# Optimization experiments

Hardware: AMD Instinct MI355X
Metric: run time of the kernel (lower is better)

## Reference

```python
import jax, jax.numpy as jnp
import numpy as np

B, N, L, H, K = 65536, 32, 8, 256, 8
RMIN, RMAX = -10.0, 10.0
MIN_BIN, MIN_SLOPE = 1e-4, 1e-4
P = 3 * K + 1  # params per feature per spline


def setup_inputs() -> dict:
    key = jax.random.key(0)
    ks = jax.random.split(key, 20)
    def rn(k, shape, s=0.05):
        return (jax.random.normal(k, shape, dtype=jnp.float32) * s)
    inp = {
        'x': jax.random.normal(ks[0], (B, N), dtype=jnp.float32),
        'sc_scale': 1.0 + rn(ks[1], (L, N)),
        'sc_shift': rn(ks[2], (L, N)),
        'W_in': rn(ks[3], (L, N, H)), 'b_in': rn(ks[4], (L, H)),
        'W1a': rn(ks[5], (L, H, H)), 'b1a': rn(ks[6], (L, H)),
        'W1b': rn(ks[7], (L, H, H)), 'b1b': rn(ks[8], (L, H)),
        'W2a': rn(ks[9], (L, H, H)), 'b2a': rn(ks[10], (L, H)),
        'W2b': rn(ks[11], (L, H, H)), 'b2b': rn(ks[12], (L, H)),
        'W_out': rn(ks[13], (L, H, N * P)), 'b_out': rn(ks[14], (L, N * P)),
        'perms': jnp.asarray(np.stack([np.random.RandomState(i).permutation(N) for i in range(L)]).astype(np.int32)),
    }
    return inp


def _conditioner(mx, Wi, bi, W1a, b1a, W1b, b1b, W2a, b2a, W2b, b2b, Wo, bo):
    # mx: [B, N] masked input -> [B, N, P] spline params
    h = mx @ Wi + bi
    r = jax.nn.relu(jax.nn.relu(h @ W1a + b1a) @ W1b + b1b)
    h = h + r
    r = jax.nn.relu(jax.nn.relu(h @ W2a + b2a) @ W2b + b2b)
    h = h + r
    h = jax.nn.relu(h)
    out = h @ Wo + bo
    return out.reshape(mx.shape[0], N, P)


def _rqs_forward(x, params):
    # x: [B, N]; params: [B, N, 3K+1]. distrax RationalQuadraticSpline forward.
    uw, uh, ud = params[..., :K], params[..., K:2 * K], params[..., 2 * K:]
    total = RMAX - RMIN
    w = jax.nn.softmax(uw, axis=-1) * (total - K * MIN_BIN) + MIN_BIN
    hgt = jax.nn.softmax(uh, axis=-1) * (total - K * MIN_BIN) + MIN_BIN
    zpad = jnp.zeros_like(w[..., :1])
    xp = RMIN + jnp.concatenate([zpad, jnp.cumsum(w, -1)], -1)   # [B,N,K+1]
    yp = RMIN + jnp.concatenate([zpad, jnp.cumsum(hgt, -1)], -1)
    offset = float(np.log(np.expm1(1.0 - MIN_SLOPE)))
    d = jax.nn.softplus(ud + offset) + MIN_SLOPE                  # [B,N,K+1]
    inside = (x > RMIN) & (x < RMAX)
    xc = jnp.clip(x, RMIN, RMAX)
    # per-element bin search (knot positions vary per element)
    idx = jnp.clip(jnp.sum((xc[..., None] >= xp).astype(jnp.int32), -1) - 1, 0, K - 1)
    g = lambda a, i: jnp.take_along_axis(a, i[..., None], -1)[..., 0]
    xk, xk1 = g(xp, idx), g(xp, idx + 1)
    yk, yk1 = g(yp, idx), g(yp, idx + 1)
    dk, dk1 = g(d, idx), g(d, idx + 1)
    bw = xk1 - xk
    bh = yk1 - yk
    s = bh / bw
    z = jnp.clip((xc - xk) / bw, 0.0, 1.0)
    zz = z * (1.0 - z)
    denom = s + (dk1 + dk - 2.0 * s) * zz
    y = yk + bh * (s * z * z + dk * zz) / denom
    ld = 2.0 * jnp.log(s) + jnp.log(dk1 * z * z + 2.0 * s * zz + dk * (1.0 - z) ** 2) - 2.0 * jnp.log(denom)
    return jnp.where(inside, y, x), jnp.where(inside, ld, 0.0)


def reference(x, sc_scale, sc_shift, W_in, b_in, W1a, b1a, W1b, b1b,
              W2a, b2a, W2b, b2b, W_out, b_out, perms):
    mask0 = (jnp.arange(N) % 2).astype(bool)  # True = identity (masked)
    logdet = jnp.zeros(x.shape[0], dtype=x.dtype)
    for i in range(L):
        # Permute
        x = x[:, perms[i]]
        # Scalar affine on all features (mask_all = all-False coupling)
        x = x * sc_scale[i] + sc_shift[i]
        logdet = logdet + jnp.sum(jnp.log(jnp.abs(sc_scale[i])))
        # RQ-spline masked coupling
        mask = mask0 if i % 2 == 0 else ~mask0
        mx = jnp.where(mask, x, 0.0)
        params = _conditioner(mx, W_in[i], b_in[i], W1a[i], b1a[i], W1b[i], b1b[i],
                              W2a[i], b2a[i], W2b[i], b2b[i], W_out[i], b_out[i])
        y, ld = _rqs_forward(x, params)
        x = jnp.where(mask, x, y)
        logdet = logdet + jnp.sum(jnp.where(mask, 0.0, ld), axis=-1)
    # standard-normal base log prob
    logp = -0.5 * jnp.sum(x * x, axis=-1) - 0.5 * N * float(np.log(2.0 * np.pi))
    return logp + logdet
```

## Files before the change

### kernel.cpp

```cpp
#include <hip/hip_runtime.h>
#include <hip/hip_bf16.h>

typedef __attribute__((ext_vector_type(8))) short bf16x8;
typedef __attribute__((ext_vector_type(16))) float f32x16;
typedef __attribute__((ext_vector_type(2))) float f32x2;

#define DEVFN __device__ __forceinline__

constexpr int NFEAT = 32, NLAYER = 8, HID = 256;
constexpr int HS  = 264;
constexpr int MXS = 40;
constexpr int XS  = 33;
constexpr int WIN_E  = 2 * 256 * 16;
constexpr int WH_E   = 16 * 256 * 16;
constexpr int WOUT_E = 16 * 512 * 16;
constexpr int LAYER_E = WIN_E + 4 * WH_E + WOUT_E;
constexpr size_t WT_BYTES = (size_t)LAYER_E * NLAYER * 2;
constexpr size_t WS_NEEDED = WT_BYTES + NLAYER * 512 * 4 + 4;

constexpr float MIN_BIN = 1e-4f, MIN_SLOPE = 1e-4f;
constexpr float SOFTPLUS_OFF = 0.5411666f;
constexpr float WSCALE = 20.0f - 8.0f * MIN_BIN;

DEVFN unsigned short bf16r(float f) {
    unsigned u = __float_as_uint(f);
    u += 0x7fffu + ((u >> 16) & 1u);
    return (unsigned short)(u >> 16);
}
#if defined(__gfx950__) && __has_builtin(__builtin_amdgcn_cvt_pk_bf16_f32)
DEVFN unsigned pack2(float a, float b) {
    auto r = __builtin_amdgcn_cvt_pk_bf16_f32(a, b);
    return __builtin_bit_cast(unsigned, r);
}
#else
DEVFN unsigned pack2(float a, float b) {
    return (unsigned)bf16r(a) | ((unsigned)bf16r(b) << 16);
}
#endif
DEVFN float bflo(unsigned v) { return __uint_as_float(v << 16); }
DEVFN float bfhi(unsigned v) { return __uint_as_float(v & 0xffff0000u); }
DEVFN float frcp(float x) { return __builtin_amdgcn_rcpf(x); }
DEVFN f32x2 vmax0(f32x2 v) {
#if __has_builtin(__builtin_elementwise_max)
    return __builtin_elementwise_max(v, (f32x2){0.f, 0.f});
#else
    return (f32x2){fmaxf(v.x, 0.f), fmaxf(v.y, 0.f)};
#endif
}

__global__ __launch_bounds__(256) void prep_kernel(
    const float* __restrict__ Win, const float* __restrict__ W1a, const float* __restrict__ W1b,
    const float* __restrict__ W2a, const float* __restrict__ W2b, const float* __restrict__ Wout,
    const float* __restrict__ bout, const float* __restrict__ scS,
    short* __restrict__ wt, float* __restrict__ bo_t, float* __restrict__ sld)
{
    __shared__ float lb[16 * 800];
    const int b = blockIdx.x, t = threadIdx.x;
    if (b < 16) {
        int l = b >> 1, ks = b & 1;
        const float* src = Win + l * 32 * 256 + ks * 16 * 256;
#pragma unroll
        for (int i = 0; i < 16; i++) { int idx = t + i * 256; lb[idx] = src[idx]; }
        __syncthreads();
        short* dst = wt + (size_t)l * LAYER_E + ks * 4096;
#pragma unroll
        for (int i = 0; i < 16; i++) {
            int o = t + i * 256; int n = o >> 4, kk = o & 15;
            dst[o] = (short)bf16r(lb[kk * 256 + n]);
        }
    } else if (b < 528) {
        int id = b - 16; int l = id >> 6, mat = (id >> 4) & 3, ks = id & 15;
        const float* mats[4] = {W1a, W1b, W2a, W2b};
        const float* src = mats[mat] + l * 65536 + ks * 16 * 256;
#pragma unroll
        for (int i = 0; i < 16; i++) { int idx = t + i * 256; lb[idx] = src[idx]; }
        __syncthreads();
        short* dst = wt + (size_t)l * LAYER_E + WIN_E + mat * WH_E + ks * 4096;
#pragma unroll
        for (int i = 0; i < 16; i++) {
            int o = t + i * 256; int n = o >> 4, kk = o & 15;
            dst[o] = (short)bf16r(lb[kk * 256 + n]);
        }
    } else if (b < 656) {
        int id = b - 528; int l = id >> 4, ks = id & 15; int par = l & 1;
        const float* src = Wout + (size_t)l * 256 * 800 + ks * 16 * 800;
        for (int k = 0; k < 16; k++)
            for (int c = t; c < 800; c += 256) lb[k * 800 + c] = src[k * 800 + c];
        __syncthreads();
        short* dst = wt + (size_t)l * LAYER_E + WIN_E + 4 * WH_E + ks * 8192;
#pragma unroll
        for (int i = 0; i < 32; i++) {
            int o = t + i * 256; int c = o >> 4, kk = o & 15;
            int u = c >> 5, p = c & 31;
            float v = (p < 25) ? lb[kk * 800 + (2 * u + par) * 25 + p] : 0.0f;
            dst[o] = (short)bf16r(v);
        }
    } else {
#pragma unroll
        for (int i = 0; i < 16; i++) {
            int idx = t + i * 256;
            int l = idx >> 9, c = idx & 511, u = c >> 5, p = c & 31;
            bo_t[idx] = (p < 25) ? bout[l * 800 + (2 * u + (l & 1)) * 25 + p] : 0.0f;
        }
        lb[t] = logf(fabsf(scS[t]));
        __syncthreads();
        for (int s = 128; s > 0; s >>= 1) { if (t < s) lb[t] += lb[t + s]; __syncthreads(); }
        if (t == 0) *sld = lb[0];
    }
}

template<int KSTEPS, int NSUB, int DEPTH>
DEVFN void gemm_flip(const short* __restrict__ wt, int ntot, int nbase,
                     const unsigned short* __restrict__ B, int bs,
                     f32x16 (&acc)[NSUB][2])
{
    constexpr int D = (KSTEPS < DEPTH) ? KSTEPS : DEPTH;
    const int lane = threadIdx.x & 63;
    const int l31 = lane & 31, l5 = lane >> 5;
    const bf16x8* __restrict__ w8 = (const bf16x8*)wt;
    const int wb = (nbase + l31) * 2 + l5;
    const int krow = ntot * 2;
    bf16x8 a[D][NSUB];
#pragma unroll
    for (int p = 0; p < D; p++)
#pragma unroll
        for (int s = 0; s < NSUB; s++) a[p][s] = w8[(size_t)p * krow + wb + s * 64];
    const unsigned short* bp = B + l31 * bs + l5 * 8;
#pragma unroll
    for (int k = 0; k < KSTEPS; k++) {
        bf16x8 b0 = *(const bf16x8*)(bp + k * 16);
        bf16x8 b1 = *(const bf16x8*)(bp + 32 * bs + k * 16);
#pragma unroll
        for (int s = 0; s < NSUB; s++) {
            acc[s][0] = __builtin_amdgcn_mfma_f32_32x32x16_bf16(a[k % D][s], b0, acc[s][0], 0, 0, 0);
            acc[s][1] = __builtin_amdgcn_mfma_f32_32x32x16_bf16(a[k % D][s], b1, acc[s][1], 0, 0, 0);
        }
        if (k + D < KSTEPS) {
#pragma unroll
            for (int s = 0; s < NSUB; s++) a[k % D][s] = w8[(size_t)(k + D) * krow + wb + s * 64];
        }
    }
}

DEVFN void binit(f32x16& a, const float* __restrict__ bias)
{
    const int q = (threadIdx.x >> 5) & 1;
    const float* bp = bias + 4 * q;
#pragma unroll
    for (int g = 0; g < 4; g++) {
        float4 b = *(const float4*)(bp + 8 * g);
        a[4*g+0] = b.x; a[4*g+1] = b.y; a[4*g+2] = b.z; a[4*g+3] = b.w;
    }
}

template<int MODE>
DEVFN void store_h(const f32x16& v, unsigned short* buf, int m0, int n0)
{
    const int lane = threadIdx.x & 63;
    const int m = m0 + (lane & 31);
    const int q = lane >> 5;
    unsigned short* rowp = buf + m * HS + n0 + 4 * q;
#pragma unroll
    for (int g = 0; g < 4; g++) {
        f32x2 r0 = {v[4*g+0], v[4*g+1]};
        f32x2 r1 = {v[4*g+2], v[4*g+3]};
        if (MODE >= 1) { r0 = vmax0(r0); r1 = vmax0(r1); }
        unsigned short* dst = rowp + 8 * g;
        if (MODE >= 2) {
            uint2 old = *(const uint2*)dst;
            r0 += (f32x2){bflo(old.x), bfhi(old.x)};
            r1 += (f32x2){bflo(old.y), bfhi(old.y)};
            if (MODE == 3) { r0 = vmax0(r0); r1 = vmax0(r1); }
        }
        uint2 pk;
        pk.x = pack2(r0.x, r0.y);
        pk.y = pack2(r1.x, r1.y);
        *(uint2*)dst = pk;
    }
}

__global__ __launch_bounds__(256, 2) void flow_kernel(
    const float* __restrict__ x_in, const float* __restrict__ scS, const float* __restrict__ scB,
    const float* __restrict__ bin, const float* __restrict__ b1a, const float* __restrict__ b1b,
    const float* __restrict__ b2a, const float* __restrict__ b2b,
    const int* __restrict__ perms,
    const short* __restrict__ wt, const float* __restrict__ bo_t, const float* __restrict__ sld,
    float* __restrict__ out)
{
    __shared__ __align__(16) unsigned short hS[64 * HS];
    __shared__ __align__(16) unsigned short uS[64 * HS];
    __shared__ float xS[64 * XS];
    __shared__ float redS[256];

    const int tid = threadIdx.x;
    const int wave = tid >> 6;
    const int lane = tid & 63;
    const int q = lane >> 5;
    const size_t rowbase = (size_t)blockIdx.x * 64;
    unsigned short* tS  = uS;
    unsigned short* mxS = uS;

#pragma unroll
    for (int i = 0; i < 8; i++) {
        int g = tid + i * 256;
        xS[(g >> 5) * XS + (g & 31)] = x_in[rowbase * NFEAT + g];
    }
    float ld_acc = 0.0f;
    __syncthreads();

    const int nbase = wave * 64;

#pragma unroll 1
    for (int l = 0; l < NLAYER; l++) {
        const int par = l & 1;
        const short* wb = wt + (size_t)l * LAYER_E;

        {
            int j = tid & 31; int r0 = (tid >> 5) * 8;
            int pj = perms[l * 32 + j];
            float sc = scS[l * 32 + j], sh = scB[l * 32 + j];
            float vals[8];
#pragma unroll
            for (int r = 0; r < 8; r++) vals[r] = xS[(r0 + r) * XS + pj] * sc + sh;
            __syncthreads();
            int keep = ((j & 1) != par);
#pragma unroll
            for (int r = 0; r < 8; r++) {
                xS[(r0 + r) * XS + j] = vals[r];
                mxS[(r0 + r) * MXS + j] = keep ? bf16r(vals[r]) : (unsigned short)0;
            }
            __syncthreads();
        }
        {
            f32x16 acc[2][2];
            binit(acc[0][0], bin + l * 256 + nbase);      binit(acc[0][1], bin + l * 256 + nbase);
            binit(acc[1][0], bin + l * 256 + nbase + 32); binit(acc[1][1], bin + l * 256 + nbase + 32);
            gemm_flip<2, 2, 2>(wb, 256, nbase, mxS, MXS, acc);
#pragma unroll
            for (int s = 0; s < 2; s++) {
                store_h<0>(acc[s][0], hS, 0,  nbase + s * 32);
                store_h<0>(acc[s][1], hS, 32, nbase + s * 32);
            }
            __syncthreads();
        }
        {
            f32x16 acc[2][2];
            binit(acc[0][0], b1a + l * 256 + nbase);      binit(acc[0][1], b1a + l * 256 + nbase);
            binit(acc[1][0], b1a + l * 256 + nbase + 32); binit(acc[1][1], b1a + l * 256 + nbase + 32);
            gemm_flip<16, 2, 4>(wb + WIN_E, 256, nbase, hS, HS, acc);
#pragma unroll
            for (int s = 0; s < 2; s++) {
                store_h<1>(acc[s][0], tS, 0,  nbase + s * 32);
                store_h<1>(acc[s][1], tS, 32, nbase + s * 32);
            }
            __syncthreads();
        }
        {
            f32x16 acc[2][2];
            binit(acc[0][0], b1b + l * 256 + nbase);      binit(acc[0][1], b1b + l * 256 + nbase);
            binit(acc[1][0], b1b + l * 256 + nbase + 32); binit(acc[1][1], b1b + l * 256 + nbase + 32);
            gemm_flip<16, 2, 4>(wb + WIN_E + WH_E, 256, nbase, tS, HS, acc);
#pragma unroll
            for (int s = 0; s < 2; s++) {
                store_h<2>(acc[s][0], hS, 0,  nbase + s * 32);
                store_h<2>(acc[s][1], hS, 32, nbase + s * 32);
            }
            __syncthreads();
        }
        {
            f32x16 acc[2][2];
            binit(acc[0][0], b2a + l * 256 + nbase);      binit(acc[0][1], b2a + l * 256 + nbase);
            binit(acc[1][0], b2a + l * 256 + nbase + 32); binit(acc[1][1], b2a + l * 256 + nbase + 32);
            gemm_flip<16, 2, 4>(wb + WIN_E + 2 * WH_E, 256, nbase, hS, HS, acc);
#pragma unroll
            for (int s = 0; s < 2; s++) {
                store_h<1>(acc[s][0], tS, 0,  nbase + s * 32);
                store_h<1>(acc[s][1], tS, 32, nbase + s * 32);
            }
            __syncthreads();
        }
        {
            f32x16 acc[2][2];
            binit(acc[0][0], b2b + l * 256 + nbase);      binit(acc[0][1], b2b + l * 256 + nbase);
            binit(acc[1][0], b2b + l * 256 + nbase + 32); binit(acc[1][1], b2b + l * 256 + nbase + 32);
            gemm_flip<16, 2, 4>(wb + WIN_E + 3 * WH_E, 256, nbase, tS, HS, acc);
#pragma unroll
            for (int s = 0; s < 2; s++) {
                store_h<3>(acc[s][0], hS, 0,  nbase + s * 32);
                store_h<3>(acc[s][1], hS, 32, nbase + s * 32);
            }
            __syncthreads();
        }
        {
            const short* wo = wb + WIN_E + 4 * WH_E;
            f32x16 acc[4][2];
            const float* bb = bo_t + l * 512 + wave * 128;
#pragma unroll
            for (int s = 0; s < 4; s++) { binit(acc[s][0], bb + s * 32); binit(acc[s][1], bb + s * 32); }
            gemm_flip<16, 4, 2>(wo, 512, wave * 128, hS, HS, acc);

#pragma unroll
            for (int s = 0; s < 4; s++) {
                float exch[16];
#pragma unroll
                for (int i = 0; i < 16; i++) {
                    float snd = q ? acc[s][0][i] : acc[s][1][i];
                    exch[i] = __shfl_xor(snd, 32, 64);
                }
                float A0[16], A1[16];
#pragma unroll
                for (int i = 0; i < 16; i++) {
                    float kept = q ? acc[s][1][i] : acc[s][0][i];
                    A0[i] = q ? exch[i] : kept;
                    A1[i] = q ? kept : exch[i];
                }
                float P[25];
#pragma unroll
                for (int p = 0; p < 25; p++) {
                    int rg = (p & 3) + 4 * (p >> 3);
                    P[p] = ((p >> 2) & 1) ? A1[rg] : A0[rg];
                }
                int n = 2 * (4 * wave + s) + par;
                float xv = xS[lane * XS + n];
                float ew[8], eh[8], sw = 0.f, sh2 = 0.f;
#pragma unroll
                for (int i = 0; i < 8; i++) { ew[i] = __expf(P[i]); sw += ew[i]; }
#pragma unroll
                for (int i = 0; i < 8; i++) { eh[i] = __expf(P[8 + i]); sh2 += eh[i]; }
                float fw = WSCALE * frcp(sw), fh = WSCALE * frcp(sh2);
                float w[8], hh[8];
#pragma unroll
                for (int i = 0; i < 8; i++) { w[i] = fmaf(ew[i], fw, MIN_BIN); hh[i] = fmaf(eh[i], fh, MIN_BIN); }

                bool inside = (xv > -10.0f) && (xv < 10.0f);
                float xc = fminf(fmaxf(xv, -10.0f), 10.0f);
                float cx = -10.0f + w[0], cy = -10.0f + hh[0];
                float xk = -10.0f, yk = -10.0f, bw = w[0], bh = hh[0];
                float udk = P[16], udk1 = P[17];
#pragma unroll
                for (int i = 1; i < 8; i++) {
                    bool take = (xc >= cx);
                    if (take) { xk = cx; yk = cy; bw = w[i]; bh = hh[i]; udk = P[16 + i]; udk1 = P[17 + i]; }
                    cx += w[i]; cy += hh[i];
                }
                float dk  = __logf(1.f + __expf(udk  + SOFTPLUS_OFF)) + MIN_SLOPE;
                float dk1 = __logf(1.f + __expf(udk1 + SOFTPLUS_OFF)) + MIN_SLOPE;
                float ibw = frcp(bw);
                float s_ = bh * ibw;
                float z = fminf(fmaxf((xc - xk) * ibw, 0.0f), 1.0f);
                float omz = 1.0f - z;
                float zz = z * omz;
                float denom = fmaf(dk1 + dk - 2.0f * s_, zz, s_);
                float idenom = frcp(denom);
                float y = fmaf(bh * fmaf(s_ * z, z, dk * zz), idenom, yk);
                float num = fmaf(dk1 * z, z, fmaf(2.0f * s_, zz, dk * omz * omz));
                float ldv = 2.0f * __logf(s_ * idenom) + __logf(num);
                xS[lane * XS + n] = inside ? y : xv;
                ld_acc += inside ? ldv : 0.0f;
            }
            __syncthreads();
        }
    }
    {
        int m = tid & 63, jg = tid >> 6;
        float s2 = 0.f;
#pragma unroll
        for (int j = 0; j < 8; j++) { float v = xS[m * XS + jg * 8 + j]; s2 += v * v; }
        redS[tid] = ld_acc - 0.5f * s2;
        __syncthreads();
        if (tid < 64) {
            float tot = redS[tid] + redS[tid + 64] + redS[tid + 128] + redS[tid + 192]
                      + *sld - 29.406033062549525f;
            out[rowbase + tid] = tot;
        }
    }
}

extern "C" void kernel_launch(void* const* d_in, const int* in_sizes, int n_in,
                              void* d_out, int out_size, void* d_ws, size_t ws_size,
                              hipStream_t stream) {
    if (ws_size < WS_NEEDED) return;
    const float* x    = (const float*)d_in[0];
    const float* scS  = (const float*)d_in[1];
    const float* scB  = (const float*)d_in[2];
    const float* Win  = (const float*)d_in[3];
    const float* bin  = (const float*)d_in[4];
    const float* W1a  = (const float*)d_in[5];
    const float* b1a  = (const float*)d_in[6];
    const float* W1b  = (const float*)d_in[7];
    const float* b1b  = (const float*)d_in[8];
    const float* W2a  = (const float*)d_in[9];
    const float* b2a  = (const float*)d_in[10];
    const float* W2b  = (const float*)d_in[11];
    const float* b2b  = (const float*)d_in[12];
    const float* Wout = (const float*)d_in[13];
    const float* bout = (const float*)d_in[14];
    const int* perms  = (const int*)d_in[15];

    short* wt   = (short*)d_ws;
    float* bo_t = (float*)((char*)d_ws + WT_BYTES);
    float* sld  = bo_t + NLAYER * 512;

    prep_kernel<<<657, 256, 0, stream>>>(Win, W1a, W1b, W2a, W2b, Wout, bout, scS, wt, bo_t, sld);
    flow_kernel<<<65536 / 64, 256, 0, stream>>>(x, scS, scB, bin, b1a, b1b, b2a, b2b,
                                                perms, wt, bo_t, sld, (float*)d_out);
}
```

Baseline: 600.0 us.

## Compose permutations, prefetch next GEMM weights across barriers, raise MFMA priority

The prep kernel now composes the per-layer feature permutations into cumulative index maps. The flow kernel then indexes x in place instead of physically permuting it, which removes a register round-trip and one block barrier per layer. Weight fragments for the next GEMM are loaded into registers before the epilogue stores and barrier of the current one, so global latency overlaps with LDS writes and synchronisation. It also uses s_setprio around the MFMA loops, a lighter barrier that waits only on LDS counters, and a single log for the log-determinant. The cost is higher register pressure from the persistent prefetch buffers, which may hurt occupancy at the 2-blocks-per-CU bound.

```diff
diff --git a/kernel.cpp b/kernel.cpp
--- a/kernel.cpp
+++ b/kernel.cpp
@@ -16,7 +16,8 @@
 constexpr int WOUT_E = 16 * 512 * 16;
 constexpr int LAYER_E = WIN_E + 4 * WH_E + WOUT_E;
 constexpr size_t WT_BYTES = (size_t)LAYER_E * NLAYER * 2;
-constexpr size_t WS_NEEDED = WT_BYTES + NLAYER * 512 * 4 + 4;
+constexpr size_t CPERM_OFF = WT_BYTES + (size_t)NLAYER * 512 * 4 + 4;
+constexpr size_t WS_NEEDED = CPERM_OFF + (size_t)NLAYER * 32 * 4;
 
 constexpr float MIN_BIN = 1e-4f, MIN_SLOPE = 1e-4f;
 constexpr float SOFTPLUS_OFF = 0.5411666f;
@@ -48,11 +49,18 @@
 #endif
 }
 
+DEVFN void bsync() {
+    asm volatile("s_waitcnt lgkmcnt(0)" ::: "memory");
+    __builtin_amdgcn_s_barrier();
+}
+
 __global__ __launch_bounds__(256) void prep_kernel(
     const float* __restrict__ Win, const float* __restrict__ W1a, const float* __restrict__ W1b,
     const float* __restrict__ W2a, const float* __restrict__ W2b, const float* __restrict__ Wout,
     const float* __restrict__ bout, const float* __restrict__ scS,
-    short* __restrict__ wt, float* __restrict__ bo_t, float* __restrict__ sld)
+    const int* __restrict__ perms,
+    short* __restrict__ wt, float* __restrict__ bo_t, float* __restrict__ sld,
+    int* __restrict__ cperm)
 {
     __shared__ float lb[16 * 800];
     const int b = blockIdx.x, t = threadIdx.x;
@@ -96,6 +104,12 @@
             dst[o] = (short)bf16r(v);
         }
     } else {
+        if (t == 0) {
+            for (int j = 0; j < 32; j++) cperm[j] = perms[j];
+            for (int l = 1; l < NLAYER; l++)
+                for (int j = 0; j < 32; j++)
+                    cperm[l * 32 + j] = cperm[(l - 1) * 32 + perms[l * 32 + j]];
+        }
 #pragma unroll
         for (int i = 0; i < 16; i++) {
             int idx = t + i * 256;
@@ -109,23 +123,32 @@
     }
 }
 
-template<int KSTEPS, int NSUB, int DEPTH>
-DEVFN void gemm_flip(const short* __restrict__ wt, int ntot, int nbase,
-                     const unsigned short* __restrict__ B, int bs,
-                     f32x16 (&acc)[NSUB][2])
-{
-    constexpr int D = (KSTEPS < DEPTH) ? KSTEPS : DEPTH;
+template<int D, int NSUB>
+DEVFN void prefA(const short* __restrict__ wt, int ntot, int nbase, bf16x8 (&a)[D][NSUB])
+{
+    const int lane = threadIdx.x & 63;
+    const bf16x8* __restrict__ w8 = (const bf16x8*)wt;
+    const int wb = (nbase + (lane & 31)) * 2 + (lane >> 5);
+    const int krow = ntot * 2;
+#pragma unroll
+    for (int p = 0; p < D; p++)
+#pragma unroll
+        for (int s = 0; s < NSUB; s++)
+            a[p][s] = w8[(size_t)p * krow + wb + s * 64];
+}
+
+template<int KSTEPS, int NSUB, int D>
+DEVFN void gemm_run(const short* __restrict__ wt, int ntot, int nbase,
+                    const unsigned short* __restrict__ B, int bs,
+                    bf16x8 (&a)[D][NSUB], f32x16 (&acc)[NSUB][2])
+{
     const int lane = threadIdx.x & 63;
     const int l31 = lane & 31, l5 = lane >> 5;
     const bf16x8* __restrict__ w8 = (const bf16x8*)wt;
     const int wb = (nbase + l31) * 2 + l5;
     const int krow = ntot * 2;
-    bf16x8 a[D][NSUB];
-#pragma unroll
-    for (int p = 0; p < D; p++)
-#pragma unroll
-        for (int s = 0; s < NSUB; s++) a[p][s] = w8[(size_t)p * krow + wb + s * 64];
     const unsigned short* bp = B + l31 * bs + l5 * 8;
+    __builtin_amdgcn_s_setprio(1);
 #pragma unroll
     for (int k = 0; k < KSTEPS; k++) {
         bf16x8 b0 = *(const bf16x8*)(bp + k * 16);
@@ -140,6 +163,7 @@
             for (int s = 0; s < NSUB; s++) a[k % D][s] = w8[(size_t)(k + D) * krow + wb + s * 64];
         }
     }
+    __builtin_amdgcn_s_setprio(0);
 }
 
 DEVFN void binit(f32x16& a, const float* __restrict__ bias)
@@ -183,7 +207,7 @@
     const float* __restrict__ x_in, const float* __restrict__ scS, const float* __restrict__ scB,
     const float* __restrict__ bin, const float* __restrict__ b1a, const float* __restrict__ b1b,
     const float* __restrict__ b2a, const float* __restrict__ b2b,
-    const int* __restrict__ perms,
+    const int* __restrict__ cperm,
     const short* __restrict__ wt, const float* __restrict__ bo_t, const float* __restrict__ sld,
     float* __restrict__ out)
 {
@@ -206,9 +230,12 @@
         xS[(g >> 5) * XS + (g & 31)] = x_in[rowbase * NFEAT + g];
     }
     float ld_acc = 0.0f;
-    __syncthreads();
+    bsync();
 
     const int nbase = wave * 64;
+    bf16x8 rG1[2][2];
+    bf16x8 rB[4][2];
+    bf16x8 rW[2][4];
 
 #pragma unroll 1
     for (int l = 0; l < NLAYER; l++) {
@@ -217,79 +244,82 @@
 
         {
             int j = tid & 31; int r0 = (tid >> 5) * 8;
-            int pj = perms[l * 32 + j];
+            int cj = cperm[l * 32 + j];
             float sc = scS[l * 32 + j], sh = scB[l * 32 + j];
-            float vals[8];
-#pragma unroll
-            for (int r = 0; r < 8; r++) vals[r] = xS[(r0 + r) * XS + pj] * sc + sh;
-            __syncthreads();
             int keep = ((j & 1) != par);
 #pragma unroll
             for (int r = 0; r < 8; r++) {
-                xS[(r0 + r) * XS + j] = vals[r];
-                mxS[(r0 + r) * MXS + j] = keep ? bf16r(vals[r]) : (unsigned short)0;
-            }
-            __syncthreads();
-        }
+                float v = fmaf(xS[(r0 + r) * XS + cj], sc, sh);
+                xS[(r0 + r) * XS + cj] = v;
+                mxS[(r0 + r) * MXS + j] = keep ? bf16r(v) : (unsigned short)0;
+            }
+        }
+        prefA<2, 2>(wb, 256, nbase, rG1);
+        bsync();
         {
             f32x16 acc[2][2];
             binit(acc[0][0], bin + l * 256 + nbase);      binit(acc[0][1], bin + l * 256 + nbase);
             binit(acc[1][0], bin + l * 256 + nbase + 32); binit(acc[1][1], bin + l * 256 + nbase + 32);
-            gemm_flip<2, 2, 2>(wb, 256, nbase, mxS, MXS, acc);
+            gemm_run<2, 2, 2>(wb, 256, nbase, mxS, MXS, rG1, acc);
+            prefA<4, 2>(wb + WIN_E, 256, nbase, rB);
 #pragma unroll
             for (int s = 0; s < 2; s++) {
                 store_h<0>(acc[s][0], hS, 0,  nbase + s * 32);
                 store_h<0>(acc[s][1], hS, 32, nbase + s * 32);
             }
-            __syncthreads();
+            bsync();
         }
         {
             f32x16 acc[2][2];
             binit(acc[0][0], b1a + l * 256 + nbase);      binit(acc[0][1], b1a + l * 256 + nbase);
             binit(acc[1][0], b1a + l * 256 + nbase + 32); binit(acc[1][1], b1a + l * 256 + nbase + 32);
-            gemm_flip<16, 2, 4>(wb + WIN_E, 256, nbase, hS, HS, acc);
+            gemm_run<16, 2, 4>(wb + WIN_E, 256, nbase, hS, HS, rB, acc);
+            prefA<4, 2>(wb + WIN_E + WH_E, 256, nbase, rB);
 #pragma unroll
             for (int s = 0; s < 2; s++) {
                 store_h<1>(acc[s][0], tS, 0,  nbase + s * 32);
                 store_h<1>(acc[s][1], tS, 32, nbase + s * 32);
             }
-            __syncthreads();
+            bsync();
         }
         {
             f32x16 acc[2][2];
             binit(acc[0][0], b1b + l * 256 + nbase);      binit(acc[0][1], b1b + l * 256 + nbase);
             binit(acc[1][0], b1b + l * 256 + nbase + 32); binit(acc[1][1], b1b + l * 256 + nbase + 32);
-            gemm_flip<16, 2, 4>(wb + WIN_E + WH_E, 256, nbase, tS, HS, acc);
+            gemm_run<16, 2, 4>(wb + WIN_E + WH_E, 256, nbase, tS, HS, rB, acc);
+            prefA<4, 2>(wb + WIN_E + 2 * WH_E, 256, nbase, rB);
 #pragma unroll
             for (int s = 0; s < 2; s++) {
                 store_h<2>(acc[s][0], hS, 0,  nbase + s * 32);
                 store_h<2>(acc[s][1], hS, 32, nbase + s * 32);
             }
-            __syncthreads();
+            bsync();
         }
         {
             f32x16 acc[2][2];
             binit(acc[0][0], b2a + l * 256 + nbase);      binit(acc[0][1], b2a + l * 256 + nbase);
             binit(acc[1][0], b2a + l * 256 + nbase + 32); binit(acc[1][1], b2a + l * 256 + nbase + 32);
-            gemm_flip<16, 2, 4>(wb + WIN_E + 2 * WH_E, 256, nbase, hS, HS, acc);
+            gemm_run<16, 2, 4>(wb + WIN_E + 2 * WH_E, 256, nbase, hS, HS, rB, acc);
+            prefA<4, 2>(wb + WIN_E + 3 * WH_E, 256, nbase, rB);
 #pragma unroll
             for (int s = 0; s < 2; s++) {
                 store_h<1>(acc[s][0], tS, 0,  nbase + s * 32);
                 store_h<1>(acc[s][1], tS, 32, nbase + s * 32);
             }
-            __syncthreads();
+            bsync();
         }
         {
             f32x16 acc[2][2];
             binit(acc[0][0], b2b + l * 256 + nbase);      binit(acc[0][1], b2b + l * 256 + nbase);
             binit(acc[1][0], b2b + l * 256 + nbase + 32); binit(acc[1][1], b2b + l * 256 + nbase + 32);
-            gemm_flip<16, 2, 4>(wb + WIN_E + 3 * WH_E, 256, nbase, tS, HS, acc);
+            gemm_run<16, 2, 4>(wb + WIN_E + 3 * WH_E, 256, nbase, tS, HS, rB, acc);
+            prefA<2, 4>(wb + WIN_E + 4 * WH_E, 512, wave * 128, rW);
 #pragma unroll
             for (int s = 0; s < 2; s++) {
                 store_h<3>(acc[s][0], hS, 0,  nbase + s * 32);
                 store_h<3>(acc[s][1], hS, 32, nbase + s * 32);
             }
-            __syncthreads();
+            bsync();
         }
         {
             const short* wo = wb + WIN_E + 4 * WH_E;
@@ -297,7 +327,7 @@
             const float* bb = bo_t + l * 512 + wave * 128;
 #pragma unroll
             for (int s = 0; s < 4; s++) { binit(acc[s][0], bb + s * 32); binit(acc[s][1], bb + s * 32); }
-            gemm_flip<16, 4, 2>(wo, 512, wave * 128, hS, HS, acc);
+            gemm_run<16, 4, 2>(wo, 512, wave * 128, hS, HS, rW, acc);
 
 #pragma unroll
             for (int s = 0; s < 4; s++) {
@@ -321,7 +351,8 @@
                     P[p] = ((p >> 2) & 1) ? A1[rg] : A0[rg];
                 }
                 int n = 2 * (4 * wave + s) + par;
-                float xv = xS[lane * XS + n];
+                int cn = cperm[l * 32 + n];
+                float xv = xS[lane * XS + cn];
                 float ew[8], eh[8], sw = 0.f, sh2 = 0.f;
 #pragma unroll
                 for (int i = 0; i < 8; i++) { ew[i] = __expf(P[i]); sw += ew[i]; }
@@ -354,11 +385,12 @@
                 float idenom = frcp(denom);
                 float y = fmaf(bh * fmaf(s_ * z, z, dk * zz), idenom, yk);
                 float num = fmaf(dk1 * z, z, fmaf(2.0f * s_, zz, dk * omz * omz));
-                float ldv = 2.0f * __logf(s_ * idenom) + __logf(num);
-                xS[lane * XS + n] = inside ? y : xv;
+                float t1 = s_ * idenom;
+                float ldv = __logf(t1 * t1 * num);
+                xS[lane * XS + cn] = inside ? y : xv;
                 ld_acc += inside ? ldv : 0.0f;
             }
-            __syncthreads();
+            bsync();
         }
     }
     {
@@ -367,7 +399,7 @@
 #pragma unroll
         for (int j = 0; j < 8; j++) { float v = xS[m * XS + jg * 8 + j]; s2 += v * v; }
         redS[tid] = ld_acc - 0.5f * s2;
-        __syncthreads();
+        bsync();
         if (tid < 64) {
             float tot = redS[tid] + redS[tid + 64] + redS[tid + 128] + redS[tid + 192]
                       + *sld - 29.406033062549525f;
@@ -400,8 +432,10 @@
     short* wt   = (short*)d_ws;
     float* bo_t = (float*)((char*)d_ws + WT_BYTES);
     float* sld  = bo_t + NLAYER * 512;
-
-    prep_kernel<<<657, 256, 0, stream>>>(Win, W1a, W1b, W2a, W2b, Wout, bout, scS, wt, bo_t, sld);
+    int* cperm  = (int*)((char*)d_ws + CPERM_OFF);
+
+    prep_kernel<<<657, 256, 0, stream>>>(Win, W1a, W1b, W2a, W2b, Wout, bout, scS, perms,
+                                         wt, bo_t, sld, cperm);
     flow_kernel<<<65536 / 64, 256, 0, stream>>>(x, scS, scB, bin, b1a, b1b, b2a, b2b,
-                                                perms, wt, bo_t, sld, (float*)d_out);
-}
+                                                cperm, wt, bo_t, sld, (float*)d_out);
+}
```

Measured after the change: 667.5 us. 1.11x slower.
